# Optimization experiments

Hardware: AMD Instinct MI355X
Metric: run time of the kernel (lower is better)

The kernel has to match this reference:

```python
import jax, jax.numpy as jnp
import numpy as np

# dims: batch, seq, embed, hidden (=4*embed), experts, top-k
B, T, D, H, E, K = 2, 4096, 1024, 4096, 8, 2


def setup_inputs() -> dict:
    key = jax.random.key(0)
    ks = jax.random.split(key, 5)
    scale = 0.02
    x = jax.random.normal(ks[0], (B, T, D), dtype=jnp.float32)
    Wr = jax.random.normal(ks[1], (D, E), dtype=jnp.float32) * scale   # router weight (no bias)
    W1 = jax.random.normal(ks[2], (E, D, H), dtype=jnp.float32) * scale  # stacked expert fc1
    b1 = jnp.zeros((E, H), dtype=jnp.float32)
    W2 = jax.random.normal(ks[3], (E, H, D), dtype=jnp.float32) * scale  # stacked expert fc2
    b2 = jnp.zeros((E, D), dtype=jnp.float32)
    return {"x": x, "Wr": Wr, "W1": W1, "b1": b1, "W2": W2, "b2": b2}


def reference(x, Wr, W1, b1, W2, b2):
    # ---- Router (eval mode: no noise) ----
    logits = jnp.einsum('btd,de->bte', x, Wr)                 # [B,T,E]
    probs = jax.nn.softmax(logits, axis=-1)
    w, idx = jax.lax.top_k(probs, K)                          # [B,T,K]
    w = w / jnp.sum(w, axis=-1, keepdims=True)                # renormalize top-k weights
    # dispatch tensor: scatter normalized weights back to expert slots
    dispatch = jnp.sum(jax.nn.one_hot(idx, E, dtype=x.dtype) * w[..., None], axis=-2)  # [B,T,E]

    # ---- Experts: each expert FFN runs densely over ALL tokens (as in source), then masked-accumulate ----
    h = jax.nn.gelu(jnp.einsum('btd,edh->ebth', x, W1) + b1[:, None, None, :], approximate=False)  # [E,B,T,H]
    y = jnp.einsum('ebth,ehd->ebtd', h, W2) + b2[:, None, None, :]                                 # [E,B,T,D]
    out = jnp.einsum('ebtd,bte->btd', y, dispatch)            # weighted accumulate over experts
    return out
```

## Files before the change

### kernel.cpp

```cpp
#include <hip/hip_runtime.h>
#include <hip/hip_bf16.h>
#include <math.h>

#define NTOK  8192
#define DD    1024
#define HH    4096
#define EE    8
#define NSLOT (NTOK*2)

typedef __attribute__((ext_vector_type(8))) short bf16x8;
typedef __attribute__((ext_vector_type(4))) float f32x4;

static __device__ __forceinline__ float gelu_exact(float v) {
    return 0.5f * v * (1.0f + erff(v * 0.70710678118654752f));
}

static __device__ __forceinline__ void gload16(const void* g, void* l) {
    __builtin_amdgcn_global_load_lds(
        (const __attribute__((address_space(1))) void*)g,
        (__attribute__((address_space(3))) void*)l, 16, 0, 0);
}

__global__ __launch_bounds__(256) void cvt_x_kernel(const float* __restrict__ x,
                                                    __hip_bfloat16* __restrict__ xb) {
    int i = (blockIdx.x * 256 + threadIdx.x) * 4;
    float4 v = *(const float4*)(x + i);
    __hip_bfloat162 lo = __float22bfloat162_rn(make_float2(v.x, v.y));
    __hip_bfloat162 hi = __float22bfloat162_rn(make_float2(v.z, v.w));
    *(__hip_bfloat162*)(xb + i)     = lo;
    *(__hip_bfloat162*)(xb + i + 2) = hi;
}

__global__ __launch_bounds__(256) void cvt_w_t_kernel(const float* __restrict__ src,
                                                      __hip_bfloat16* __restrict__ dst,
                                                      int R, int C) {
    __shared__ float tile[32][33];
    int e = blockIdx.z;
    size_t base = (size_t)e * R * C;
    int c0 = blockIdx.x * 32, r0 = blockIdx.y * 32;
    int tx = threadIdx.x, ty = threadIdx.y;
    #pragma unroll
    for (int q = 0; q < 4; ++q)
        tile[ty + q * 8][tx] = src[base + (size_t)(r0 + ty + q * 8) * C + (c0 + tx)];
    __syncthreads();
    #pragma unroll
    for (int q = 0; q < 4; ++q)
        dst[base + (size_t)(c0 + ty + q * 8) * R + (r0 + tx)] =
            __float2bfloat16(tile[tx][ty + q * 8]);
}

__global__ __launch_bounds__(256) void router_kernel(const float* __restrict__ x,
                                                     const float* __restrict__ Wr,
                                                     int* __restrict__ topk_idx,
                                                     float* __restrict__ topk_w,
                                                     int* __restrict__ counts) {
    __shared__ float wr[DD * 9];
    for (int i = threadIdx.x; i < DD * EE; i += 256) {
        int d = i >> 3, e = i & 7;
        wr[d * 9 + e] = Wr[i];
    }
    __syncthreads();
    int wave = threadIdx.x >> 6, lane = threadIdx.x & 63;
    int t = blockIdx.x * 4 + wave;
    const float* xr = x + (size_t)t * DD;
    float acc[EE] = {};
    for (int j = 0; j < DD / 64; ++j) {
        float v = xr[j * 64 + lane];
        int d = j * 64 + lane;
        #pragma unroll
        for (int e = 0; e < EE; ++e) acc[e] += v * wr[d * 9 + e];
    }
    #pragma unroll
    for (int off = 32; off > 0; off >>= 1)
        #pragma unroll
        for (int e = 0; e < EE; ++e) acc[e] += __shfl_xor(acc[e], off);
    if (lane == 0) {
        int e1 = 0;
        #pragma unroll
        for (int e = 1; e < EE; ++e) if (acc[e] > acc[e1]) e1 = e;
        int e2 = (e1 == 0) ? 1 : 0;
        #pragma unroll
        for (int e = 0; e < EE; ++e)
            if (e != e1 && e != e2 && acc[e] > acc[e2]) e2 = e;
        float w1 = 1.0f / (1.0f + expf(acc[e2] - acc[e1]));
        topk_idx[t * 2]     = e1;
        topk_idx[t * 2 + 1] = e2;
        topk_w[t * 2]       = w1;
        topk_w[t * 2 + 1]   = 1.0f - w1;
        atomicAdd(&counts[e1], 1);
        atomicAdd(&counts[e2], 1);
    }
}

__global__ void prefix_kernel(const int* __restrict__ counts,
                              int* __restrict__ offsets, int* __restrict__ cursors) {
    if (threadIdx.x == 0 && blockIdx.x == 0) {
        int s = 0;
        for (int e = 0; e < EE; ++e) { offsets[e] = s; cursors[e] = s; s += counts[e]; }
        offsets[EE] = s;
    }
}

__global__ __launch_bounds__(256) void scatter_kernel(const int* __restrict__ topk_idx,
                                                      int* __restrict__ cursors,
                                                      int* __restrict__ btok,
                                                      int* __restrict__ slot_of) {
    int t = blockIdx.x * 256 + threadIdx.x;
    if (t >= NTOK) return;
    #pragma unroll
    for (int k = 0; k < 2; ++k) {
        int e = topk_idx[t * 2 + k];
        int p = atomicAdd(&cursors[e], 1);
        btok[p] = t;
        slot_of[t * 2 + k] = p;
    }
}

__global__ __launch_bounds__(256) void fc1_kernel(
    const __hip_bfloat16* __restrict__ xb, const __hip_bfloat16* __restrict__ w1t,
    const float* __restrict__ b1g, const int* __restrict__ offsets,
    const int* __restrict__ btok, __hip_bfloat16* __restrict__ hbuf,
    int h0, int Cchunk) {
    int e = blockIdx.z;
    int seg0 = offsets[e];
    int cnt  = offsets[e + 1] - seg0;
    int m0 = blockIdx.y * 128;
    if (m0 >= cnt) return;
    int n0 = h0 + blockIdx.x * 128;

    __shared__ __align__(16) __hip_bfloat16 As[128 * 32];
    __shared__ __align__(16) __hip_bfloat16 Bs[128 * 32];

    int tid = threadIdx.x;
    int wv = tid >> 6, lane = tid & 63;
    int lr  = lane >> 2;
    int lcq = lane & 3;

    int ra0 = wv * 32 + lr;
    int ra1 = ra0 + 16;
    int ga0 = m0 + ra0, ga1 = m0 + ra1;
    int tok0 = btok[seg0 + (ga0 < cnt ? ga0 : 0)];
    int tok1 = btok[seg0 + (ga1 < cnt ? ga1 : 0)];
    const __hip_bfloat16* a0 = xb + (size_t)tok0 * DD + lcq * 8;
    const __hip_bfloat16* a1 = xb + (size_t)tok1 * DD + lcq * 8;
    const __hip_bfloat16* b0 = w1t + ((size_t)e * HH + n0 + ra0) * DD + lcq * 8;
    const __hip_bfloat16* b1p = w1t + ((size_t)e * HH + n0 + ra1) * DD + lcq * 8;
    __hip_bfloat16* lA0 = As + (wv * 32) * 32;
    __hip_bfloat16* lA1 = As + (wv * 32 + 16) * 32;
    __hip_bfloat16* lB0 = Bs + (wv * 32) * 32;
    __hip_bfloat16* lB1 = Bs + (wv * 32 + 16) * 32;

    int wr_ = wv >> 1, wc = wv & 1;
    int q = lane >> 4, lc = lane & 15;

    f32x4 acc[4][4] = {};

    for (int k0 = 0; k0 < DD; k0 += 32) {
        gload16(a0 + k0, lA0);
        gload16(a1 + k0, lA1);
        gload16(b0 + k0, lB0);
        gload16(b1p + k0, lB1);
        __syncthreads();
        bf16x8 af[4], bg[4];
        #pragma unroll
        for (int i = 0; i < 4; ++i)
            af[i] = *(const bf16x8*)(As + (wr_ * 64 + i * 16 + lc) * 32 + q * 8);
        #pragma unroll
        for (int j = 0; j < 4; ++j)
            bg[j] = *(const bf16x8*)(Bs + (wc * 64 + j * 16 + lc) * 32 + q * 8);
        #pragma unroll
        for (int i = 0; i < 4; ++i)
            #pragma unroll
            for (int j = 0; j < 4; ++j)
                acc[i][j] = __builtin_amdgcn_mfma_f32_16x16x32_bf16(af[i], bg[j], acc[i][j], 0, 0, 0);
        __syncthreads();
    }

    #pragma unroll
    for (int i = 0; i < 4; ++i) {
        #pragma unroll
        for (int j = 0; j < 4; ++j) {
            int col = n0 + wc * 64 + j * 16 + lc;
            float bias = b1g[e * HH + col];
            #pragma unroll
            for (int rg = 0; rg < 4; ++rg) {
                int ml = wr_ * 64 + i * 16 + q * 4 + rg;
                if (m0 + ml < cnt) {
                    float v = acc[i][j][rg] + bias;
                    hbuf[(size_t)(seg0 + m0 + ml) * Cchunk + (col - h0)] =
                        __float2bfloat16(gelu_exact(v));
                }
            }
        }
    }
}

__global__ __launch_bounds__(256) void fc2_kernel(
    const __hip_bfloat16* __restrict__ hbuf, const __hip_bfloat16* __restrict__ w2t,
    const int* __restrict__ offsets, float* __restrict__ ybuf,
    int h0, int Cchunk) {
    int e = blockIdx.z;
    int seg0 = offsets[e];
    int cnt  = offsets[e + 1] - seg0;
    int m0 = blockIdx.y * 128;
    if (m0 >= cnt) return;
    int n0 = blockIdx.x * 128;

    __shared__ __align__(16) __hip_bfloat16 As[128 * 32];
    __shared__ __align__(16) __hip_bfloat16 Bs[128 * 32];

    int tid = threadIdx.x;
    int wv = tid >> 6, lane = tid & 63;
    int lr  = lane >> 2;
    int lcq = lane & 3;

    int ra0 = wv * 32 + lr;
    int ra1 = ra0 + 16;
    int ga0 = m0 + ra0, ga1 = m0 + ra1;
    int slot0 = seg0 + (ga0 < cnt ? ga0 : 0);
    int slot1 = seg0 + (ga1 < cnt ? ga1 : 0);
    const __hip_bfloat16* a0 = hbuf + (size_t)slot0 * Cchunk + lcq * 8;
    const __hip_bfloat16* a1 = hbuf + (size_t)slot1 * Cchunk + lcq * 8;
    const __hip_bfloat16* b0 = w2t + ((size_t)e * DD + n0 + ra0) * HH + h0 + lcq * 8;
    const __hip_bfloat16* b1p = w2t + ((size_t)e * DD + n0 + ra1) * HH + h0 + lcq * 8;
    __hip_bfloat16* lA0 = As + (wv * 32) * 32;
    __hip_bfloat16* lA1 = As + (wv * 32 + 16) * 32;
    __hip_bfloat16* lB0 = Bs + (wv * 32) * 32;
    __hip_bfloat16* lB1 = Bs + (wv * 32 + 16) * 32;

    int wr_ = wv >> 1, wc = wv & 1;
    int q = lane >> 4, lc = lane & 15;

    f32x4 acc[4][4] = {};

    for (int k0 = 0; k0 < Cchunk; k0 += 32) {
        gload16(a0 + k0, lA0);
        gload16(a1 + k0, lA1);
        gload16(b0 + k0, lB0);
        gload16(b1p + k0, lB1);
        __syncthreads();
        bf16x8 af[4], bg[4];
        #pragma unroll
        for (int i = 0; i < 4; ++i)
            af[i] = *(const bf16x8*)(As + (wr_ * 64 + i * 16 + lc) * 32 + q * 8);
        #pragma unroll
        for (int j = 0; j < 4; ++j)
            bg[j] = *(const bf16x8*)(Bs + (wc * 64 + j * 16 + lc) * 32 + q * 8);
        #pragma unroll
        for (int i = 0; i < 4; ++i)
            #pragma unroll
            for (int j = 0; j < 4; ++j)
                acc[i][j] = __builtin_amdgcn_mfma_f32_16x16x32_bf16(af[i], bg[j], acc[i][j], 0, 0, 0);
        __syncthreads();
    }

    #pragma unroll
    for (int i = 0; i < 4; ++i) {
        #pragma unroll
        for (int j = 0; j < 4; ++j) {
            int col = n0 + wc * 64 + j * 16 + lc;
            #pragma unroll
            for (int rg = 0; rg < 4; ++rg) {
                int ml = wr_ * 64 + i * 16 + q * 4 + rg;
                if (m0 + ml < cnt) {
                    size_t yi = (size_t)(seg0 + m0 + ml) * DD + col;
                    float v = acc[i][j][rg];
                    ybuf[yi] = (h0 == 0) ? v : (ybuf[yi] + v);
                }
            }
        }
    }
}

__global__ __launch_bounds__(256) void combine_kernel(
    const float* __restrict__ ybuf, const float* __restrict__ b2,
    const int* __restrict__ topk_idx, const float* __restrict__ topk_w,
    const int* __restrict__ slot_of, float* __restrict__ out) {
    int idx = blockIdx.x * 256 + threadIdx.x;
    int t  = idx >> 8;
    int d4 = (idx & 255) * 4;
    int e0 = topk_idx[t * 2], e1 = topk_idx[t * 2 + 1];
    float w0 = topk_w[t * 2], w1 = topk_w[t * 2 + 1];
    int s0 = slot_of[t * 2], s1 = slot_of[t * 2 + 1];
    float4 y0 = *(const float4*)(ybuf + (size_t)s0 * DD + d4);
    float4 y1 = *(const float4*)(ybuf + (size_t)s1 * DD + d4);
    float4 c0 = *(const float4*)(b2 + e0 * DD + d4);
    float4 c1 = *(const float4*)(b2 + e1 * DD + d4);
    float4 o;
    o.x = w0 * (y0.x + c0.x) + w1 * (y1.x + c1.x);
    o.y = w0 * (y0.y + c0.y) + w1 * (y1.y + c1.y);
    o.z = w0 * (y0.z + c0.z) + w1 * (y1.z + c1.z);
    o.w = w0 * (y0.w + c0.w) + w1 * (y1.w + c1.w);
    *(float4*)(out + (size_t)t * DD + d4) = o;
}

static inline size_t alignup(size_t v, size_t a) { return (v + a - 1) & ~(a - 1); }

extern "C" void kernel_launch(void* const* d_in, const int* in_sizes, int n_in,
                              void* d_out, int out_size, void* d_ws, size_t ws_size,
                              hipStream_t stream) {
    const float* x  = (const float*)d_in[0];
    const float* Wr = (const float*)d_in[1];
    const float* W1 = (const float*)d_in[2];
    const float* b1 = (const float*)d_in[3];
    const float* W2 = (const float*)d_in[4];
    const float* b2 = (const float*)d_in[5];
    float* out = (float*)d_out;

    char* p = (char*)d_ws;
    size_t off = 0;
    int* counts  = (int*)(p + off); off += 64;
    int* offsets = (int*)(p + off); off += 64;
    int* cursors = (int*)(p + off); off += 64;
    off = alignup(off, 256);
    int*   topk_idx = (int*)(p + off);   off += (size_t)NTOK * 2 * 4;
    float* topk_w   = (float*)(p + off); off += (size_t)NTOK * 2 * 4;
    int*   btok     = (int*)(p + off);   off += (size_t)NSLOT * 4;
    int*   slot_of  = (int*)(p + off);   off += (size_t)NTOK * 2 * 4;
    off = alignup(off, 256);
    __hip_bfloat16* xb  = (__hip_bfloat16*)(p + off); off += (size_t)NTOK * DD * 2;
    __hip_bfloat16* w1t = (__hip_bfloat16*)(p + off); off += (size_t)EE * DD * HH * 2;
    __hip_bfloat16* w2t = (__hip_bfloat16*)(p + off); off += (size_t)EE * DD * HH * 2;
    float* ybuf = (float*)(p + off);                  off += (size_t)NSLOT * DD * 4;
    off = alignup(off, 256);
    __hip_bfloat16* hbuf = (__hip_bfloat16*)(p + off);
    size_t rem = (ws_size > off) ? (ws_size - off) : 0;
    int C = HH;
    while (C > 128 && (size_t)NSLOT * C * 2 > rem) C >>= 1;

    hipMemsetAsync(counts, 0, 192, stream);

    cvt_x_kernel<<<NTOK * DD / 1024, 256, 0, stream>>>(x, xb);
    cvt_w_t_kernel<<<dim3(HH / 32, DD / 32, EE), dim3(32, 8), 0, stream>>>(W1, w1t, DD, HH);
    cvt_w_t_kernel<<<dim3(DD / 32, HH / 32, EE), dim3(32, 8), 0, stream>>>(W2, w2t, HH, DD);
    router_kernel<<<NTOK / 4, 256, 0, stream>>>(x, Wr, topk_idx, topk_w, counts);
    prefix_kernel<<<1, 64, 0, stream>>>(counts, offsets, cursors);
    scatter_kernel<<<NTOK / 256, 256, 0, stream>>>(topk_idx, cursors, btok, slot_of);

    for (int h0 = 0; h0 < HH; h0 += C) {
        fc1_kernel<<<dim3(C / 128, NTOK / 128, EE), 256, 0, stream>>>(
            xb, w1t, b1, offsets, btok, hbuf, h0, C);
        fc2_kernel<<<dim3(DD / 128, NTOK / 128, EE), 256, 0, stream>>>(
            hbuf, w2t, offsets, ybuf, h0, C);
    }
    combine_kernel<<<NTOK * DD / 4 / 256, 256, 0, stream>>>(
        ybuf, b2, topk_idx, topk_w, slot_of, out);
}
```

Measured before the change: 1.139 ms.

## Double K-step per barrier and swizzle grouped-GEMM block order across experts

Both expert GEMM kernels now load two 32-wide K slices per iteration into doubled LDS buffers, halving the number of barrier pairs per tile. The 3D grid is flattened to 1D, and block indices are decoded with a swizzle that groups 8 consecutive (expert, m-tile) pairs per n-tile. The aim is to cut sync overhead and to interleave blocks across experts so that weight and activation tiles are reused in cache. The cost is doubled LDS per block, which may lower occupancy, and a 1D launch in which many blocks exit early.

```diff
diff --git a/kernel.cpp b/kernel.cpp
--- a/kernel.cpp
+++ b/kernel.cpp
@@ -7,6 +7,8 @@
 #define HH    4096
 #define EE    8
 #define NSLOT (NTOK*2)
+#define MY    (NTOK/128)
+#define EM    (EE*MY)
 
 typedef __attribute__((ext_vector_type(8))) short bf16x8;
 typedef __attribute__((ext_vector_type(4))) float f32x4;
@@ -19,6 +21,17 @@
     __builtin_amdgcn_global_load_lds(
         (const __attribute__((address_space(1))) void*)g,
         (__attribute__((address_space(3))) void*)l, 16, 0, 0);
+}
+
+static __device__ __forceinline__ void decode_swizzle(int flat, int NX,
+                                                      int& e, int& m, int& n) {
+    int r = flat & 7;
+    int t = flat >> 3;
+    n = t % NX;
+    int q = t / NX;
+    int em = q * 8 + r;
+    e = em >> 6;
+    m = em & 63;
 }
 
 __global__ __launch_bounds__(256) void cvt_x_kernel(const float* __restrict__ x,
@@ -120,16 +133,17 @@
     const __hip_bfloat16* __restrict__ xb, const __hip_bfloat16* __restrict__ w1t,
     const float* __restrict__ b1g, const int* __restrict__ offsets,
     const int* __restrict__ btok, __hip_bfloat16* __restrict__ hbuf,
-    int h0, int Cchunk) {
-    int e = blockIdx.z;
+    int h0, int Cchunk, int NX) {
+    int e, m, n;
+    decode_swizzle(blockIdx.x, NX, e, m, n);
     int seg0 = offsets[e];
     int cnt  = offsets[e + 1] - seg0;
-    int m0 = blockIdx.y * 128;
+    int m0 = m * 128;
     if (m0 >= cnt) return;
-    int n0 = h0 + blockIdx.x * 128;
-
-    __shared__ __align__(16) __hip_bfloat16 As[128 * 32];
-    __shared__ __align__(16) __hip_bfloat16 Bs[128 * 32];
+    int n0 = h0 + n * 128;
+
+    __shared__ __align__(16) __hip_bfloat16 As[2 * 128 * 32];
+    __shared__ __align__(16) __hip_bfloat16 Bs[2 * 128 * 32];
 
     int tid = threadIdx.x;
     int wv = tid >> 6, lane = tid & 63;
@@ -155,24 +169,31 @@
 
     f32x4 acc[4][4] = {};
 
-    for (int k0 = 0; k0 < DD; k0 += 32) {
+    for (int k0 = 0; k0 < DD; k0 += 64) {
         gload16(a0 + k0, lA0);
         gload16(a1 + k0, lA1);
         gload16(b0 + k0, lB0);
         gload16(b1p + k0, lB1);
+        gload16(a0 + k0 + 32, lA0 + 4096);
+        gload16(a1 + k0 + 32, lA1 + 4096);
+        gload16(b0 + k0 + 32, lB0 + 4096);
+        gload16(b1p + k0 + 32, lB1 + 4096);
         __syncthreads();
-        bf16x8 af[4], bg[4];
-        #pragma unroll
-        for (int i = 0; i < 4; ++i)
-            af[i] = *(const bf16x8*)(As + (wr_ * 64 + i * 16 + lc) * 32 + q * 8);
-        #pragma unroll
-        for (int j = 0; j < 4; ++j)
-            bg[j] = *(const bf16x8*)(Bs + (wc * 64 + j * 16 + lc) * 32 + q * 8);
-        #pragma unroll
-        for (int i = 0; i < 4; ++i)
+        #pragma unroll
+        for (int h = 0; h < 2; ++h) {
+            bf16x8 af[4], bg[4];
+            #pragma unroll
+            for (int i = 0; i < 4; ++i)
+                af[i] = *(const bf16x8*)(As + h * 4096 + (wr_ * 64 + i * 16 + lc) * 32 + q * 8);
             #pragma unroll
             for (int j = 0; j < 4; ++j)
-                acc[i][j] = __builtin_amdgcn_mfma_f32_16x16x32_bf16(af[i], bg[j], acc[i][j], 0, 0, 0);
+                bg[j] = *(const bf16x8*)(Bs + h * 4096 + (wc * 64 + j * 16 + lc) * 32 + q * 8);
+            #pragma unroll
+            for (int i = 0; i < 4; ++i)
+                #pragma unroll
+                for (int j = 0; j < 4; ++j)
+                    acc[i][j] = __builtin_amdgcn_mfma_f32_16x16x32_bf16(af[i], bg[j], acc[i][j], 0, 0, 0);
+        }
         __syncthreads();
     }
 
@@ -199,15 +220,16 @@
     const __hip_bfloat16* __restrict__ hbuf, const __hip_bfloat16* __restrict__ w2t,
     const int* __restrict__ offsets, float* __restrict__ ybuf,
     int h0, int Cchunk) {
-    int e = blockIdx.z;
+    int e, m, n;
+    decode_swizzle(blockIdx.x, DD / 128, e, m, n);
     int seg0 = offsets[e];
     int cnt  = offsets[e + 1] - seg0;
-    int m0 = blockIdx.y * 128;
+    int m0 = m * 128;
     if (m0 >= cnt) return;
-    int n0 = blockIdx.x * 128;
-
-    __shared__ __align__(16) __hip_bfloat16 As[128 * 32];
-    __shared__ __align__(16) __hip_bfloat16 Bs[128 * 32];
+    int n0 = n * 128;
+
+    __shared__ __align__(16) __hip_bfloat16 As[2 * 128 * 32];
+    __shared__ __align__(16) __hip_bfloat16 Bs[2 * 128 * 32];
 
     int tid = threadIdx.x;
     int wv = tid >> 6, lane = tid & 63;
@@ -233,24 +255,31 @@
 
     f32x4 acc[4][4] = {};
 
-    for (int k0 = 0; k0 < Cchunk; k0 += 32) {
+    for (int k0 = 0; k0 < Cchunk; k0 += 64) {
         gload16(a0 + k0, lA0);
         gload16(a1 + k0, lA1);
         gload16(b0 + k0, lB0);
         gload16(b1p + k0, lB1);
+        gload16(a0 + k0 + 32, lA0 + 4096);
+        gload16(a1 + k0 + 32, lA1 + 4096);
+        gload16(b0 + k0 + 32, lB0 + 4096);
+        gload16(b1p + k0 + 32, lB1 + 4096);
         __syncthreads();
-        bf16x8 af[4], bg[4];
-        #pragma unroll
-        for (int i = 0; i < 4; ++i)
-            af[i] = *(const bf16x8*)(As + (wr_ * 64 + i * 16 + lc) * 32 + q * 8);
-        #pragma unroll
-        for (int j = 0; j < 4; ++j)
-            bg[j] = *(const bf16x8*)(Bs + (wc * 64 + j * 16 + lc) * 32 + q * 8);
-        #pragma unroll
-        for (int i = 0; i < 4; ++i)
+        #pragma unroll
+        for (int h = 0; h < 2; ++h) {
+            bf16x8 af[4], bg[4];
+            #pragma unroll
+            for (int i = 0; i < 4; ++i)
+                af[i] = *(const bf16x8*)(As + h * 4096 + (wr_ * 64 + i * 16 + lc) * 32 + q * 8);
             #pragma unroll
             for (int j = 0; j < 4; ++j)
-                acc[i][j] = __builtin_amdgcn_mfma_f32_16x16x32_bf16(af[i], bg[j], acc[i][j], 0, 0, 0);
+                bg[j] = *(const bf16x8*)(Bs + h * 4096 + (wc * 64 + j * 16 + lc) * 32 + q * 8);
+            #pragma unroll
+            for (int i = 0; i < 4; ++i)
+                #pragma unroll
+                for (int j = 0; j < 4; ++j)
+                    acc[i][j] = __builtin_amdgcn_mfma_f32_16x16x32_bf16(af[i], bg[j], acc[i][j], 0, 0, 0);
+        }
         __syncthreads();
     }
 
@@ -338,9 +367,10 @@
     scatter_kernel<<<NTOK / 256, 256, 0, stream>>>(topk_idx, cursors, btok, slot_of);
 
     for (int h0 = 0; h0 < HH; h0 += C) {
-        fc1_kernel<<<dim3(C / 128, NTOK / 128, EE), 256, 0, stream>>>(
-            xb, w1t, b1, offsets, btok, hbuf, h0, C);
-        fc2_kernel<<<dim3(DD / 128, NTOK / 128, EE), 256, 0, stream>>>(
+        int nx1 = C / 128;
+        fc1_kernel<<<EM * nx1, 256, 0, stream>>>(
+            xb, w1t, b1, offsets, btok, hbuf, h0, C, nx1);
+        fc2_kernel<<<EM * (DD / 128), 256, 0, stream>>>(
             hbuf, w2t, offsets, ybuf, h0, C);
     }
     combine_kernel<<<NTOK * DD / 4 / 256, 256, 0, stream>>>(
```

Result: slower. 1.278 ms (+12.2%).
